# Kernel tuning notes

Hardware: AMD Instinct MI355X
Metric: run time of the kernel (lower is better)

## Reference

```python
import jax, jax.numpy as jnp
import numpy as np

N_NODES = 10000
W_DIM = 512
N_EDGES = 200000


def setup_inputs() -> dict:
    key = jax.random.key(0)
    k1, k2, k3 = jax.random.split(key, 3)
    z_drug = jax.random.normal(k1, (N_NODES, W_DIM), dtype=jnp.float32)
    # glorot-style init for the bilinear weight
    glorot_std = jnp.sqrt(2.0 / (W_DIM + W_DIM)).astype(jnp.float32)
    weight = jax.random.normal(k2, (W_DIM, W_DIM), dtype=jnp.float32) * glorot_std
    batch_edges = jax.random.randint(k3, (2, N_EDGES), 0, N_NODES, dtype=jnp.int64)
    return {"z_drug": z_drug, "weight": weight, "batch_edges": batch_edges}


def reference(z_drug, weight, batch_edges):
    # edge_type == 'drug_drug': both endpoints come from the drug table.
    row_embed = z_drug[batch_edges[0]]  # [E, d]
    col_embed = z_drug[batch_edges[1]]  # [E, d]
    # score_e = row_e @ W @ col_e  == diag((Z1 W) Z2^T) without the N x N blowup
    score = jnp.einsum('ed,df,ef->e', row_embed, weight, col_embed)
    return jax.nn.sigmoid(score)  # is_sigmoid=True default
```

## Files before the change

kernel.cpp:

```cpp
#include <hip/hip_runtime.h>
#include <math.h>

#define DIM     512
#define NNODES  10000
#define NEDGES  200000
#define MPAD    10048
#define NMB     157
#define NGRP    5
#define NB      (NGRP * NNODES)
#define SCAN_BLK 49

using short8  = __attribute__((ext_vector_type(8))) short;
using floatx4 = __attribute__((ext_vector_type(4))) float;
using half8   = __attribute__((ext_vector_type(8))) _Float16;
using half2v  = __attribute__((ext_vector_type(2))) _Float16;

__device__ inline float dot2acc(half2v a, half2v b, float c) {
#if __has_builtin(__builtin_amdgcn_fdot2)
    return __builtin_amdgcn_fdot2(a, b, c, false);
#else
    return fmaf((float)a[0], (float)b[0], fmaf((float)a[1], (float)b[1], c));
#endif
}

#define PREP_ZBLK 2512
__global__ __launch_bounds__(256) void prep(const float* __restrict__ Z,
                                            const float* __restrict__ W,
                                            _Float16* __restrict__ Zh16,
                                            _Float16* __restrict__ Wh16t,
                                            int* __restrict__ counts) {
    const int b = blockIdx.x;
    const int t = threadIdx.x;

    if (b < 196) {
        int i = b * 256 + t;
        if (i < NB) counts[i] = 0;
    }

    if (b < PREP_ZBLK) {
        const int idx8 = (b * 256 + t) * 8;
        const int m = idx8 >> 9;
        float x[8];
        if (m < NNODES) {
            float4 v0 = *(const float4*)(Z + idx8);
            float4 v1 = *(const float4*)(Z + idx8 + 4);
            x[0]=v0.x; x[1]=v0.y; x[2]=v0.z; x[3]=v0.w;
            x[4]=v1.x; x[5]=v1.y; x[6]=v1.z; x[7]=v1.w;
        } else {
            #pragma unroll
            for (int j = 0; j < 8; ++j) x[j] = 0.f;
        }
        half8 h;
        #pragma unroll
        for (int j = 0; j < 8; ++j) h[j] = (_Float16)x[j];
        *(half8*)(Zh16 + idx8) = h;
    } else {
        __shared__ float tile[64][65];
        const int wb = b - PREP_ZBLK;
        const int kb = (wb >> 3) * 64;
        const int nb = (wb & 7) * 64;
        const int kk = t >> 2;
        const int ch = t & 3;

        const float* src = W + (size_t)(kb + kk) * DIM + nb + ch * 16;
        #pragma unroll
        for (int q = 0; q < 4; ++q) {
            float4 v = *(const float4*)(src + q * 4);
            tile[kk][ch * 16 + q * 4 + 0] = v.x;
            tile[kk][ch * 16 + q * 4 + 1] = v.y;
            tile[kk][ch * 16 + q * 4 + 2] = v.z;
            tile[kk][ch * 16 + q * 4 + 3] = v.w;
        }
        __syncthreads();

        const int nn = kk;
        half8 h0, h1;
        #pragma unroll
        for (int i = 0; i < 8; ++i) h0[i] = (_Float16)tile[ch * 16 + i][nn];
        #pragma unroll
        for (int i = 0; i < 8; ++i) h1[i] = (_Float16)tile[ch * 16 + 8 + i][nn];
        _Float16* d = Wh16t + (size_t)(nb + nn) * DIM + kb + ch * 16;
        *(half8*)(d)     = h0;
        *(half8*)(d + 8) = h1;
    }
}

__global__ __launch_bounds__(256) void gemm_f16(const _Float16* __restrict__ Zh16,
                                                const _Float16* __restrict__ Wh16t,
                                                _Float16* __restrict__ ZWh) {
    __shared__ _Float16 Abuf[2][64 * 32];
    __shared__ _Float16 Bbuf[2][128 * 32];

    const int t     = threadIdx.x;
    const int bid   = blockIdx.x;
    const int n_idx = bid & 3;
    const int m0    = (bid >> 2) * 64;
    const int n0    = n_idx * 128;

    const int l  = t & 63;
    const int w  = t >> 6;
    const int wn = w * 32;
    const int lm = l & 15;
    const int lq = l >> 4;
    const unsigned wbase = (unsigned)(t & 192);

    floatx4 acc[4][2] = {};

    const int arow = t >> 2;
    const int ach  = t & 3;

    auto stage = [&](int buf, int k0) {
        {
            const _Float16* s = Zh16 + (size_t)(m0 + arow) * DIM + k0 + ach * 8;
            __builtin_amdgcn_global_load_lds(
                (const __attribute__((address_space(1))) void*)s,
                (__attribute__((address_space(3))) void*)&Abuf[buf][wbase * 8], 16, 0, 0);
        }
        #pragma unroll
        for (int p = 0; p < 2; ++p) {
            const int sidx = p * 256 + t;
            const int row  = sidx >> 2;
            const int ch   = sidx & 3;
            const _Float16* s = Wh16t + (size_t)(n0 + row) * DIM + k0 + ch * 8;
            __builtin_amdgcn_global_load_lds(
                (const __attribute__((address_space(1))) void*)s,
                (__attribute__((address_space(3))) void*)&Bbuf[buf][(p * 256 + wbase) * 8], 16, 0, 0);
        }
    };

    stage(0, 0);
    __syncthreads();

    for (int s = 0; s < 16; ++s) {
        const int buf = s & 1;
        if (s < 15) stage(buf ^ 1, (s + 1) * 32);

        half8 aF[4], bF[2];
        #pragma unroll
        for (int i = 0; i < 4; ++i)
            aF[i] = *(const half8*)&Abuf[buf][(16 * i + lm) * 32 + lq * 8];
        #pragma unroll
        for (int j = 0; j < 2; ++j)
            bF[j] = *(const half8*)&Bbuf[buf][(wn + 16 * j + lm) * 32 + lq * 8];

        #pragma unroll
        for (int i = 0; i < 4; ++i)
            #pragma unroll
            for (int j = 0; j < 2; ++j)
                acc[i][j] = __builtin_amdgcn_mfma_f32_16x16x32_f16(aF[i], bF[j], acc[i][j], 0, 0, 0);

        __syncthreads();
    }

    #pragma unroll
    for (int i = 0; i < 4; ++i)
        #pragma unroll
        for (int j = 0; j < 2; ++j)
            #pragma unroll
            for (int r = 0; r < 4; ++r) {
                const int gm = m0 + 16 * i + lq * 4 + r;
                const int gn = n0 + wn + 16 * j + lm;
                if (gm < NNODES)
                    ZWh[(size_t)gm * DIM + gn] = (_Float16)acc[i][j][r];
            }
}

__global__ void hist_rows(const int* __restrict__ eidx, int* __restrict__ counts) {
    int e = blockIdx.x * blockDim.x + threadIdx.x;
    if (e < NEDGES) {
        int r = eidx[e];
        int c = eidx[NEDGES + e];
        atomicAdd(&counts[(c >> 11) * NNODES + r], 1);
    }
}

__global__ __launch_bounds__(1024) void scan_local(const int* __restrict__ counts,
                                                   int* __restrict__ partial,
                                                   int* __restrict__ blksum) {
    __shared__ int wsum[16];
    __shared__ int woff[17];
    const int t    = threadIdx.x;
    const int lane = t & 63;
    const int wv   = t >> 6;
    const int i    = blockIdx.x * 1024 + t;

    int x = (i < NB) ? counts[i] : 0;

    int v = x;
    #pragma unroll
    for (int off = 1; off < 64; off <<= 1) {
        int u = __shfl_up(v, off, 64);
        if (lane >= off) v += u;
    }
    if (lane == 63) wsum[wv] = v;
    __syncthreads();
    if (t == 0) {
        int r = 0;
        #pragma unroll
        for (int k = 0; k < 16; ++k) { woff[k] = r; r += wsum[k]; }
        woff[16] = r;
    }
    __syncthreads();

    if (i < NB) partial[i] = woff[wv] + (v - x);
    if (t == 1023) blksum[blockIdx.x] = woff[16];
}

__global__ __launch_bounds__(1024) void scan_fix(const int* __restrict__ partial,
                                                 const int* __restrict__ blksum,
                                                 int* __restrict__ cursor) {
    __shared__ int base_s;
    const int t = threadIdx.x;
    const int b = blockIdx.x;

    if (t < 64) {
        int v = (t < b) ? blksum[t] : 0;
        #pragma unroll
        for (int off = 32; off > 0; off >>= 1)
            v += __shfl_xor(v, off, 64);
        if (t == 0) base_s = v;
    }
    __syncthreads();
    const int base = base_s;

    const int i = b * 1024 + t;
    if (i < NB)
        cursor[i] = base + partial[i];
}

__global__ void scatter_edges(const int* __restrict__ eidx,
                              int* __restrict__ cursor,
                              unsigned* __restrict__ keys,
                              unsigned short* __restrict__ rows16) {
    int e = blockIdx.x * blockDim.x + threadIdx.x;
    if (e < NEDGES) {
        int r = eidx[e];
        int c = eidx[NEDGES + e];
        int pos = atomicAdd(&cursor[(c >> 11) * NNODES + r], 1);
        keys[pos]   = ((unsigned)c << 18) | (unsigned)e;
        rows16[pos] = (unsigned short)r;
    }
}

__global__ __launch_bounds__(256) void edge_score_f(const _Float16* __restrict__ ZWh,
                                                    const _Float16* __restrict__ Zh,
                                                    const unsigned* __restrict__ keys,
                                                    const unsigned short* __restrict__ rows16,
                                                    float* __restrict__ out) {
    const int t    = threadIdx.x;
    const int wgid = blockIdx.x * 4 + (t >> 6);
    const int lane = t & 63;
    const int gq   = lane >> 4;
    const int sl   = lane & 15;

    const int ii = wgid * 4 + gq;
    const unsigned k = keys[ii];
    const int c = (int)(k >> 18);
    const int r = (int)rows16[ii];

    const _Float16* rp = ZWh + (size_t)r * DIM + sl * 32;
    const _Float16* cp = Zh  + (size_t)c * DIM + sl * 32;

    half8 ra0 = *(const half8*)(rp);
    half8 ra1 = *(const half8*)(rp + 8);
    half8 ra2 = *(const half8*)(rp + 16);
    half8 ra3 = *(const half8*)(rp + 24);
    half8 c0  = *(const half8*)(cp);
    half8 c1  = *(const half8*)(cp + 8);
    half8 c2  = *(const half8*)(cp + 16);
    half8 c3  = *(const half8*)(cp + 24);

    float s = 0.f;
    #pragma unroll
    for (int d = 0; d < 4; ++d) {
        s = dot2acc((half2v){ra0[2*d], ra0[2*d+1]}, (half2v){c0[2*d], c0[2*d+1]}, s);
        s = dot2acc((half2v){ra1[2*d], ra1[2*d+1]}, (half2v){c1[2*d], c1[2*d+1]}, s);
        s = dot2acc((half2v){ra2[2*d], ra2[2*d+1]}, (half2v){c2[2*d], c2[2*d+1]}, s);
        s = dot2acc((half2v){ra3[2*d], ra3[2*d+1]}, (half2v){c3[2*d], c3[2*d+1]}, s);
    }

    s += __shfl_xor(s, 1, 64);
    s += __shfl_xor(s, 2, 64);
    s += __shfl_xor(s, 4, 64);
    s += __shfl_xor(s, 8, 64);

    if (sl == 0)
        out[k & 0x3FFFFu] = 1.0f / (1.0f + expf(-s));
}

#define GTM 128
#define GTN 64
#define GTK 16
#define LDA 132
#define LDB 68

__global__ __launch_bounds__(256) void gemm_zw(const float* __restrict__ A,
                                               const float* __restrict__ B,
                                               float* __restrict__ C) {
    __shared__ float As[GTK * LDA];
    __shared__ float Bs[GTK * LDB];

    const int t  = threadIdx.x;
    const int m0 = blockIdx.x * GTM;
    const int n0 = blockIdx.y * GTN;
    const int tx = t & 15;
    const int ty = t >> 4;

    float acc[8][4] = {};

    for (int k0 = 0; k0 < DIM; k0 += GTK) {
        #pragma unroll
        for (int p = 0; p < 2; ++p) {
            int f  = t + p * 256;
            int mm = f >> 2;
            int kq = f & 3;
            int m  = m0 + mm;
            float4 v = make_float4(0.f, 0.f, 0.f, 0.f);
            if (m < NNODES)
                v = *(const float4*)(A + (size_t)m * DIM + k0 + kq * 4);
            As[(kq * 4 + 0) * LDA + mm] = v.x;
            As[(kq * 4 + 1) * LDA + mm] = v.y;
            As[(kq * 4 + 2) * LDA + mm] = v.z;
            As[(kq * 4 + 3) * LDA + mm] = v.w;
        }
        {
            int kb = t >> 4, n4 = t & 15;
            *(float4*)&Bs[kb * LDB + n4 * 4] =
                *(const float4*)(B + (size_t)(k0 + kb) * DIM + n0 + n4 * 4);
        }
        __syncthreads();

        #pragma unroll
        for (int kk = 0; kk < GTK; ++kk) {
            float4 a0 = *(const float4*)&As[kk * LDA + ty * 8];
            float4 a1 = *(const float4*)&As[kk * LDA + ty * 8 + 4];
            float4 b  = *(const float4*)&Bs[kk * LDB + tx * 4];
            float av[8] = {a0.x, a0.y, a0.z, a0.w, a1.x, a1.y, a1.z, a1.w};
            float bv[4] = {b.x, b.y, b.z, b.w};
            #pragma unroll
            for (int i = 0; i < 8; ++i)
                #pragma unroll
                for (int j = 0; j < 4; ++j)
                    acc[i][j] = fmaf(av[i], bv[j], acc[i][j]);
        }
        __syncthreads();
    }

    #pragma unroll
    for (int i = 0; i < 8; ++i) {
        int m = m0 + ty * 8 + i;
        if (m < NNODES)
            *(float4*)(C + (size_t)m * DIM + n0 + tx * 4) =
                make_float4(acc[i][0], acc[i][1], acc[i][2], acc[i][3]);
    }
}

__global__ __launch_bounds__(256) void edge_score(const float* __restrict__ ZW,
                                                  const float* __restrict__ Z,
                                                  const int* __restrict__ eidx,
                                                  float* __restrict__ out) {
    const int e    = blockIdx.x * 4 + (threadIdx.x >> 6);
    const int lane = threadIdx.x & 63;

    const int r = eidx[e];
    const int c = eidx[NEDGES + e];

    const float4* pr = (const float4*)(ZW + (size_t)r * DIM);
    const float4* pc = (const float4*)(Z  + (size_t)c * DIM);

    float4 a0 = pr[lane * 2 + 0];
    float4 a1 = pr[lane * 2 + 1];
    float4 b0 = pc[lane * 2 + 0];
    float4 b1 = pc[lane * 2 + 1];

    float s = a0.x * b0.x;
    s = fmaf(a0.y, b0.y, s);
    s = fmaf(a0.z, b0.z, s);
    s = fmaf(a0.w, b0.w, s);
    s = fmaf(a1.x, b1.x, s);
    s = fmaf(a1.y, b1.y, s);
    s = fmaf(a1.z, b1.z, s);
    s = fmaf(a1.w, b1.w, s);

    #pragma unroll
    for (int off = 32; off > 0; off >>= 1)
        s += __shfl_xor(s, off, 64);

    if (lane == 0)
        out[e] = 1.0f / (1.0f + expf(-s));
}

extern "C" void kernel_launch(void* const* d_in, const int* in_sizes, int n_in,
                              void* d_out, int out_size, void* d_ws, size_t ws_size,
                              hipStream_t stream) {
    const float* Z  = (const float*)d_in[0];
    const float* W  = (const float*)d_in[1];
    const int*   EI = (const int*)d_in[2];
    float* out = (float*)d_out;

    char* p = (char*)d_ws;
    _Float16* ZWh   = (_Float16*)p;  p += (size_t)MPAD * DIM * 2;
    _Float16* Zh16  = (_Float16*)p;  p += (size_t)MPAD * DIM * 2;
    _Float16* Wh16t = (_Float16*)p;  p += (size_t)DIM * DIM * 2;
    int* counts  = (int*)p;          p += (size_t)NB * 4;
    int* cursor  = (int*)p;          p += (size_t)NB * 4;
    int* partial = (int*)p;          p += (size_t)NB * 4;
    int* blksum  = (int*)p;          p += (size_t)SCAN_BLK * 4;
    unsigned* keys = (unsigned*)p;   p += (size_t)NEDGES * 4;
    unsigned short* rows16 = (unsigned short*)p; p += (size_t)NEDGES * 2;
    const size_t need_full = (size_t)(p - (char*)d_ws);

    if (ws_size >= need_full) {
        prep<<<PREP_ZBLK + 64, 256, 0, stream>>>(Z, W, Zh16, Wh16t, counts);
        gemm_f16<<<NMB * 4, 256, 0, stream>>>(Zh16, Wh16t, ZWh);
        hist_rows<<<(NEDGES + 255) / 256, 256, 0, stream>>>(EI, counts);
        scan_local<<<SCAN_BLK, 1024, 0, stream>>>(counts, partial, blksum);
        scan_fix<<<SCAN_BLK, 1024, 0, stream>>>(partial, blksum, cursor);
        scatter_edges<<<(NEDGES + 255) / 256, 256, 0, stream>>>(EI, cursor, keys, rows16);
        edge_score_f<<<NEDGES / 16, 256, 0, stream>>>(ZWh, Zh16, keys, rows16, out);
    } else {
        float* ZW = (float*)d_ws;
        dim3 g1((NNODES + GTM - 1) / GTM, DIM / GTN);
        gemm_zw<<<g1, 256, 0, stream>>>(Z, W, ZW);
        edge_score<<<NEDGES / 4, 256, 0, stream>>>(ZW, Z, EI, out);
    }
}
```

Baseline: 140.1 us.

## Fuse edge histogram into GEMM kernel and double K-step per stage

The separate hist_rows launch is removed. Its atomic histogram work now runs as a grid-stride loop at the tail of each GEMM block, which saves one kernel launch and the dependency gap that came with it. The GEMM also stages 64 K-elements per pipeline step instead of 32. That halves the number of barriers and loop iterations but doubles the shared memory per block, which may reduce occupancy. The atomics now run after the GEMM epilogue in every block, which adds tail latency to the GEMM.

```diff
diff --git a/kernel.cpp b/kernel.cpp
--- a/kernel.cpp
+++ b/kernel.cpp
@@ -9,6 +9,7 @@
 #define NGRP    5
 #define NB      (NGRP * NNODES)
 #define SCAN_BLK 49
+#define GEMM_GRID (NMB * 4)
 
 using short8  = __attribute__((ext_vector_type(8))) short;
 using floatx4 = __attribute__((ext_vector_type(4))) float;
@@ -87,9 +88,11 @@
 
 __global__ __launch_bounds__(256) void gemm_f16(const _Float16* __restrict__ Zh16,
                                                 const _Float16* __restrict__ Wh16t,
-                                                _Float16* __restrict__ ZWh) {
-    __shared__ _Float16 Abuf[2][64 * 32];
-    __shared__ _Float16 Bbuf[2][128 * 32];
+                                                _Float16* __restrict__ ZWh,
+                                                const int* __restrict__ eidx,
+                                                int* __restrict__ counts) {
+    __shared__ _Float16 Abuf[2][2 * 64 * 32];
+    __shared__ _Float16 Bbuf[2][2 * 128 * 32];
 
     const int t     = threadIdx.x;
     const int bid   = blockIdx.x;
@@ -106,48 +109,56 @@
 
     floatx4 acc[4][2] = {};
 
-    const int arow = t >> 2;
-    const int ach  = t & 3;
-
     auto stage = [&](int buf, int k0) {
-        {
-            const _Float16* s = Zh16 + (size_t)(m0 + arow) * DIM + k0 + ach * 8;
+        #pragma unroll
+        for (int p = 0; p < 2; ++p) {
+            const int s   = p * 256 + t;
+            const int kk  = s >> 8;
+            const int row = (s >> 2) & 63;
+            const int ch  = s & 3;
+            const _Float16* src = Zh16 + (size_t)(m0 + row) * DIM + k0 + kk * 32 + ch * 8;
             __builtin_amdgcn_global_load_lds(
-                (const __attribute__((address_space(1))) void*)s,
-                (__attribute__((address_space(3))) void*)&Abuf[buf][wbase * 8], 16, 0, 0);
-        }
-        #pragma unroll
-        for (int p = 0; p < 2; ++p) {
-            const int sidx = p * 256 + t;
-            const int row  = sidx >> 2;
-            const int ch   = sidx & 3;
-            const _Float16* s = Wh16t + (size_t)(n0 + row) * DIM + k0 + ch * 8;
+                (const __attribute__((address_space(1))) void*)src,
+                (__attribute__((address_space(3))) void*)&Abuf[buf][(p * 256 + wbase) * 8],
+                16, 0, 0);
+        }
+        #pragma unroll
+        for (int p = 0; p < 4; ++p) {
+            const int s   = p * 256 + t;
+            const int kk  = s >> 9;
+            const int row = (s >> 2) & 127;
+            const int ch  = s & 3;
+            const _Float16* src = Wh16t + (size_t)(n0 + row) * DIM + k0 + kk * 32 + ch * 8;
             __builtin_amdgcn_global_load_lds(
-                (const __attribute__((address_space(1))) void*)s,
-                (__attribute__((address_space(3))) void*)&Bbuf[buf][(p * 256 + wbase) * 8], 16, 0, 0);
+                (const __attribute__((address_space(1))) void*)src,
+                (__attribute__((address_space(3))) void*)&Bbuf[buf][(p * 256 + wbase) * 8],
+                16, 0, 0);
         }
     };
 
     stage(0, 0);
     __syncthreads();
 
-    for (int s = 0; s < 16; ++s) {
+    for (int s = 0; s < 8; ++s) {
         const int buf = s & 1;
-        if (s < 15) stage(buf ^ 1, (s + 1) * 32);
-
-        half8 aF[4], bF[2];
-        #pragma unroll
-        for (int i = 0; i < 4; ++i)
-            aF[i] = *(const half8*)&Abuf[buf][(16 * i + lm) * 32 + lq * 8];
-        #pragma unroll
-        for (int j = 0; j < 2; ++j)
-            bF[j] = *(const half8*)&Bbuf[buf][(wn + 16 * j + lm) * 32 + lq * 8];
-
-        #pragma unroll
-        for (int i = 0; i < 4; ++i)
+        if (s < 7) stage(buf ^ 1, (s + 1) * 64);
+
+        #pragma unroll
+        for (int kk = 0; kk < 2; ++kk) {
+            half8 aF[4], bF[2];
+            #pragma unroll
+            for (int i = 0; i < 4; ++i)
+                aF[i] = *(const half8*)&Abuf[buf][kk * 2048 + (16 * i + lm) * 32 + lq * 8];
             #pragma unroll
             for (int j = 0; j < 2; ++j)
-                acc[i][j] = __builtin_amdgcn_mfma_f32_16x16x32_f16(aF[i], bF[j], acc[i][j], 0, 0, 0);
+                bF[j] = *(const half8*)&Bbuf[buf][kk * 4096 + (wn + 16 * j + lm) * 32 + lq * 8];
+
+            #pragma unroll
+            for (int i = 0; i < 4; ++i)
+                #pragma unroll
+                for (int j = 0; j < 2; ++j)
+                    acc[i][j] = __builtin_amdgcn_mfma_f32_16x16x32_f16(aF[i], bF[j], acc[i][j], 0, 0, 0);
+        }
 
         __syncthreads();
     }
@@ -163,11 +174,8 @@
                 if (gm < NNODES)
                     ZWh[(size_t)gm * DIM + gn] = (_Float16)acc[i][j][r];
             }
-}
-
-__global__ void hist_rows(const int* __restrict__ eidx, int* __restrict__ counts) {
-    int e = blockIdx.x * blockDim.x + threadIdx.x;
-    if (e < NEDGES) {
+
+    for (int e = bid * 256 + t; e < NEDGES; e += GEMM_GRID * 256) {
         int r = eidx[e];
         int c = eidx[NEDGES + e];
         atomicAdd(&counts[(c >> 11) * NNODES + r], 1);
@@ -412,8 +420,7 @@
 
     if (ws_size >= need_full) {
         prep<<<PREP_ZBLK + 64, 256, 0, stream>>>(Z, W, Zh16, Wh16t, counts);
-        gemm_f16<<<NMB * 4, 256, 0, stream>>>(Zh16, Wh16t, ZWh);
-        hist_rows<<<(NEDGES + 255) / 256, 256, 0, stream>>>(EI, counts);
+        gemm_f16<<<GEMM_GRID, 256, 0, stream>>>(Zh16, Wh16t, ZWh, EI, counts);
         scan_local<<<SCAN_BLK, 1024, 0, stream>>>(counts, partial, blksum);
         scan_fix<<<SCAN_BLK, 1024, 0, stream>>>(partial, blksum, cursor);
         scatter_edges<<<(NEDGES + 255) / 256, 256, 0, stream>>>(EI, cursor, keys, rows16);
```

Result: faster. 135.8 us (-3.1%).
